# Kernel optimization log

Hardware: AMD Instinct MI355X
Metric: run time of the kernel (lower is better)

## Reference

```python
import jax, jax.numpy as jnp
from jax import lax
import numpy as np


def conv(x, w, b):
    # x: [N,C,H,W], w: [O,I,kh,kw] (torch layout), VALID padding, stride 1
    y = lax.conv_general_dilated(x, w, (1, 1), 'VALID',
                                 dimension_numbers=('NCHW', 'OIHW', 'NCHW'))
    return y + b[None, :, None, None]


def prelu4(x, a):
    return jnp.where(x > 0, x, a[None, :, None, None] * x)


def prelu1(x, a):
    return jnp.where(x > 0, x, a * x)


def maxpool_ceil(x, k, s):
    # torch MaxPool2d(k, s, ceil_mode=True): pad right/bottom so last partial window counts
    def pad_amt(n):
        out = -(-(n - k) // s) + 1  # ceil((n-k)/s)+1
        return max((out - 1) * s + k - n, 0)
    ph, pw = pad_amt(x.shape[2]), pad_amt(x.shape[3])
    return lax.reduce_window(x, -jnp.inf, lax.max, (1, 1, k, k), (1, 1, s, s),
                             [(0, 0), (0, 0), (0, ph), (0, pw)])


def setup_inputs() -> dict:
    key = jax.random.key(0)
    ks = iter(jax.random.split(key, 64))
    def rn(shape, s=0.05):
        return jax.random.normal(next(ks), shape, dtype=jnp.float32) * s
    p = {}
    p['imgs'] = rn((8, 3, 720, 720), 1.0)
    p['crops24'] = rn((2048, 3, 24, 24), 1.0)
    p['crops48'] = rn((512, 3, 48, 48), 1.0)
    # PNet
    p['pw1'] = rn((10, 3, 3, 3)); p['pb1'] = rn((10,)); p['pa1'] = jnp.full((10,), 0.25, jnp.float32)
    p['pw2'] = rn((16, 10, 3, 3)); p['pb2'] = rn((16,)); p['pa2'] = jnp.full((16,), 0.25, jnp.float32)
    p['pw3'] = rn((32, 16, 3, 3)); p['pb3'] = rn((32,)); p['pa3'] = jnp.full((32,), 0.25, jnp.float32)
    p['pw41'] = rn((2, 32, 1, 1)); p['pb41'] = rn((2,))
    p['pw42'] = rn((4, 32, 1, 1)); p['pb42'] = rn((4,))
    # RNet
    p['rw1'] = rn((28, 3, 3, 3)); p['rb1'] = rn((28,)); p['ra1'] = jnp.full((28,), 0.25, jnp.float32)
    p['rw2'] = rn((48, 28, 3, 3)); p['rb2'] = rn((48,)); p['ra2'] = jnp.full((48,), 0.25, jnp.float32)
    p['rw3'] = rn((64, 48, 2, 2)); p['rb3'] = rn((64,)); p['ra3'] = jnp.full((64,), 0.25, jnp.float32)
    p['rd4w'] = rn((128, 576)); p['rd4b'] = rn((128,)); p['ra4'] = jnp.full((128,), 0.25, jnp.float32)
    p['rd51w'] = rn((2, 128)); p['rd51b'] = rn((2,))
    p['rd52w'] = rn((4, 128)); p['rd52b'] = rn((4,))
    # ONet
    p['ow1'] = rn((32, 3, 3, 3)); p['ob1'] = rn((32,)); p['oa1'] = jnp.full((32,), 0.25, jnp.float32)
    p['ow2'] = rn((64, 32, 3, 3)); p['ob2'] = rn((64,)); p['oa2'] = jnp.full((64,), 0.25, jnp.float32)
    p['ow3'] = rn((64, 64, 3, 3)); p['ob3'] = rn((64,)); p['oa3'] = jnp.full((64,), 0.25, jnp.float32)
    p['ow4'] = rn((128, 64, 2, 2)); p['ob4'] = rn((128,)); p['oa4'] = jnp.full((128,), 0.25, jnp.float32)
    p['od5w'] = rn((256, 1152)); p['od5b'] = rn((256,)); p['oa5'] = jnp.full((256,), 0.25, jnp.float32)
    p['od61w'] = rn((2, 256)); p['od61b'] = rn((2,))
    p['od62w'] = rn((4, 256)); p['od62b'] = rn((4,))
    p['od63w'] = rn((10, 256)); p['od63b'] = rn((10,))
    return p


def reference(imgs, crops24, crops48,
              pw1, pb1, pa1, pw2, pb2, pa2, pw3, pb3, pa3, pw41, pb41, pw42, pb42,
              rw1, rb1, ra1, rw2, rb2, ra2, rw3, rb3, ra3, rd4w, rd4b, ra4,
              rd51w, rd51b, rd52w, rd52b,
              ow1, ob1, oa1, ow2, ob2, oa2, ow3, ob3, oa3, ow4, ob4, oa4,
              od5w, od5b, oa5, od61w, od61b, od62w, od62b, od63w, od63b):
    # --- PNet (fully convolutional, stage 1) ---
    x = prelu4(conv(imgs, pw1, pb1), pa1)
    x = maxpool_ceil(x, 2, 2)
    x = prelu4(conv(x, pw2, pb2), pa2)
    x = prelu4(conv(x, pw3, pb3), pa3)
    p_prob = jax.nn.softmax(conv(x, pw41, pb41), axis=1)  # [B,2,Hp,Wp]
    p_reg = conv(x, pw42, pb42)                            # [B,4,Hp,Wp]
    # --- RNet (24x24 crops, stage 2) ---
    x = prelu4(conv(crops24, rw1, rb1), ra1)
    x = maxpool_ceil(x, 3, 2)
    x = prelu4(conv(x, rw2, rb2), ra2)
    x = maxpool_ceil(x, 3, 2)
    x = prelu4(conv(x, rw3, rb3), ra3)
    x = jnp.transpose(x, (0, 3, 2, 1)).reshape(x.shape[0], -1)  # permute(0,3,2,1).view
    x = prelu1(x @ rd4w.T + rd4b, ra4)
    r_a = jax.nn.softmax(x @ rd51w.T + rd51b, axis=1)  # [N,2]
    r_b = x @ rd52w.T + rd52b                           # [N,4]
    # --- ONet (48x48 crops, stage 3) ---
    x = prelu4(conv(crops48, ow1, ob1), oa1)
    x = maxpool_ceil(x, 3, 2)
    x = prelu4(conv(x, ow2, ob2), oa2)
    x = maxpool_ceil(x, 3, 2)
    x = prelu4(conv(x, ow3, ob3), oa3)
    x = maxpool_ceil(x, 2, 2)
    x = prelu4(conv(x, ow4, ob4), oa4)
    x = jnp.transpose(x, (0, 3, 2, 1)).reshape(x.shape[0], -1)
    x = prelu1(x @ od5w.T + od5b, oa5)
    o_a = jax.nn.softmax(x @ od61w.T + od61b, axis=1)  # [M,2]
    o_b = x @ od62w.T + od62b                           # [M,4]
    o_c = x @ od63w.T + od63b                           # [M,10]
    return (p_reg, p_prob, r_b, r_a, o_b, o_c, o_a)
```

## Files before the change

### kernel.cpp

```cpp
#include <hip/hip_runtime.h>
#include <hip/hip_bf16.h>

typedef __hip_bfloat16 bf16;
typedef unsigned short u16;
typedef unsigned int u32;

typedef float f32x16 __attribute__((ext_vector_type(16)));
typedef short s16x8 __attribute__((ext_vector_type(8)));

__device__ __forceinline__ float b2f(bf16 v) { return __bfloat162float(v); }
__device__ __forceinline__ bf16  f2b(float v) { return __float2bfloat16(v); }
__device__ __forceinline__ float us2f(u16 u) { return __uint_as_float((u32)u << 16); }
__device__ __forceinline__ float ulo(u32 u)  { return __uint_as_float(u << 16); }
__device__ __forceinline__ float uhi(u32 u)  { return __uint_as_float(u & 0xFFFF0000u); }

#define OFF_IMGS 0
#define OFF_C24  12441600
#define OFF_C48  15980544
#define OFF_WTS  19519488
#define OFF_A    20119488
#define OFF_B    54819488
#define OFF_RW   71319488
#define RW_RC2   (OFF_RW)
#define RW_RC3   (OFF_RW + 18432)
#define RW_OC2   (OFF_RW + 30720)
#define RW_OC3   (OFF_RW + 49152)
#define RW_OC4   (OFF_RW + 86016)
#define ARENA_N  (OFF_RW + 118784L)

__device__ bf16 g_arena[ARENA_N];
__device__ int  g_isf32;

__global__ void detect_kern(const void* imgs)
{
    if (threadIdx.x != 0) return;
    const u16* u = (const u16*)imgs;
    int f32 = 0;
    for (int i = 0; i < 256; ++i) {
        int e = (u[i] >> 7) & 0xFF;
        if (e >= 0x8D) f32 = 1;
    }
    g_isf32 = f32;
}

__global__ void convert_kern(const void* __restrict__ src, int dst_off, int n)
{
    int i = blockIdx.x * blockDim.x + threadIdx.x;
    if (i >= n) return;
    float v = g_isf32 ? ((const float*)src)[i] : b2f(((const bf16*)src)[i]);
    g_arena[(long)dst_off + i] = f2b(v);
}

struct CvtEnt { const void* src; int dst_off; int n; };
struct CvtTab { CvtEnt e[50]; };
__global__ void convert_many_kern(CvtTab tab)
{
    CvtEnt ent = tab.e[blockIdx.y];
    int i = blockIdx.x * blockDim.x + threadIdx.x;
    if (i >= ent.n) return;
    float v = g_isf32 ? ((const float*)ent.src)[i] : b2f(((const bf16*)ent.src)[i]);
    g_arena[(long)ent.dst_off + i] = f2b(v);
}

__device__ __forceinline__ void stout(void* base, long idx, float v, int f32)
{
    if (f32) ((float*)base)[idx] = v;
    else     ((bf16*)base)[idx] = f2b(v);
}

__global__ void repack_w_kern(int w_off, int rw_off, int CO, int CIN, int CPAD,
                              int KHW, int total)
{
    int i = blockIdx.x * blockDim.x + threadIdx.x;
    if (i >= total) return;
    int c = i % CPAD;
    int t = i / CPAD;
    int g = t % KHW;
    int o = t / KHW;
    u16 v = 0;
    if (o < CO && c < CIN)
        v = ((const u16*)g_arena)[w_off + ((long)(o * CIN + c)) * KHW + g];
    ((u16*)g_arena)[(long)rw_off + i] = v;
}

template<int CIN,int KH,int KW,int H,int W,int OH,int OW,int CO,int OBLK,int R>
__launch_bounds__(256)
__global__ void conv_a_kern(int in_off, int w_off, int b_off, int a_off, int out_off)
{
    constexpr int KTOT = CIN * KH * KW;
    constexpr int INCNT = CIN * H * W;
    constexpr int OPT = OBLK / 8;
    constexpr int NPX = OH * OW;
    constexpr int PBLK = 32 * R;
    __shared__ __align__(16) u16 in_s[INCNT];
    __shared__ __align__(16) u16 w_s[KTOT * OBLK];
    __shared__ __align__(16) u16 out_s[PBLK * CO];

    int n = blockIdx.x, pxc = blockIdx.y;
    const u16* ga = (const u16*)g_arena;

    const u32* src = (const u32*)(ga + in_off + (long)n * INCNT);
    u32* dst = (u32*)in_s;
    for (int i = threadIdx.x; i < INCNT / 2; i += 256) dst[i] = src[i];
    for (int i = threadIdx.x; i < KTOT * OBLK; i += 256) {
        int o_l = i % OBLK, k = i / OBLK;
        w_s[i] = (o_l < CO) ? ga[w_off + (long)o_l * KTOT + k] : (u16)0;
    }
    __syncthreads();

    int lane = threadIdx.x & 31, og = threadIdx.x >> 5;
    int pixoff[R];
    bool vld[R];
    #pragma unroll
    for (int r = 0; r < R; ++r) {
        int px = pxc * PBLK + lane + r * 32;
        vld[r] = px < NPX;
        int p = vld[r] ? px : 0;
        pixoff[r] = (p / OW) * W + (p % OW);
    }
    float acc[R][OPT];
    #pragma unroll
    for (int r = 0; r < R; ++r)
        #pragma unroll
        for (int j = 0; j < OPT; ++j) acc[r][j] = 0.f;

    const u32* wu = (const u32*)w_s;
    for (int c = 0; c < CIN; ++c) {
        #pragma unroll
        for (int ky = 0; ky < KH; ++ky) {
            #pragma unroll
            for (int kx = 0; kx < KW; ++kx) {
                int k = (c * KH + ky) * KW + kx;
                int ub = c * (H * W) + ky * W + kx;
                float a[R];
                #pragma unroll
                for (int r = 0; r < R; ++r) a[r] = us2f(in_s[ub + pixoff[r]]);
                int wb = (k * OBLK + og * OPT) >> 1;
                float wv[OPT];
                #pragma unroll
                for (int jj = 0; jj < OPT / 2; ++jj) {
                    u32 u = wu[wb + jj];
                    wv[2 * jj] = ulo(u); wv[2 * jj + 1] = uhi(u);
                }
                #pragma unroll
                for (int r = 0; r < R; ++r)
                    #pragma unroll
                    for (int j = 0; j < OPT; ++j)
                        acc[r][j] += a[r] * wv[j];
            }
        }
    }
    #pragma unroll
    for (int j = 0; j < OPT; ++j) {
        int o = og * OPT + j;
        if (o < CO) {
            float b = us2f(ga[b_off + o]);
            float al = us2f(ga[a_off + o]);
            #pragma unroll
            for (int r = 0; r < R; ++r) if (vld[r]) {
                float v = acc[r][j] + b;
                v = v > 0.f ? v : v * al;
                u16 bits; bf16 t = f2b(v); __builtin_memcpy(&bits, &t, 2);
                out_s[(lane + r * 32) * CO + o] = bits;
            }
        }
    }
    __syncthreads();
    int base_px = pxc * PBLK;
    int npx_blk = NPX - base_px; if (npx_blk > PBLK) npx_blk = PBLK;
    int tot8 = (npx_blk * CO) >> 3;
    uint4* gout = (uint4*)&g_arena[(long)out_off + ((long)n * NPX + base_px) * CO];
    const uint4* osrc = (const uint4*)out_s;
    for (int i = threadIdx.x; i < tot8; i += 256) gout[i] = osrc[i];
}

template<int CIN,int CPAD,int KH,int KW,int H,int W,int OH,int OW,int CO,int NT>
__launch_bounds__(256, 2)
__global__ void conv_mfma_kern(int in_off, int rw_off, int b_off, int a_off, int out_off)
{
    constexpr int NPX = OH * OW;
    constexpr int MT = (NPX + 31) / 32;
    constexpr int PST = CPAD + 8;
    constexpr int NCH = CPAD / 16;
    constexpr int KHW = KH * KW;
    constexpr int NG = KHW * NCH;
    __shared__ __align__(16) u16 patchT[H * W * PST];

    int n = blockIdx.x;
    const u16* ga = (const u16*)g_arena;
    const u16* in = ga + in_off + (long)n * (H * W * CIN);

    if constexpr (CIN == CPAD) {
        constexpr int NV = H * W * (CPAD / 8);
        for (int i = threadIdx.x; i < NV; i += 256) {
            int pix = i / (CPAD / 8), j = i % (CPAD / 8);
            *(s16x8*)&patchT[pix * PST + j * 8] = *(const s16x8*)&in[pix * CPAD + j * 8];
        }
    } else {
        constexpr int TOT = H * W * CPAD;
        for (int i = threadIdx.x; i < TOT; i += 256) {
            int pix = i / CPAD, c = i % CPAD;
            patchT[pix * PST + c] = (c < CIN) ? in[pix * CIN + c] : (u16)0;
        }
    }
    __syncthreads();

    int m = threadIdx.x & 31, half = (threadIdx.x >> 5) & 1, wave = threadIdx.x >> 6;
    int c0 = half * 8;
    int nt = wave % NT;
    int o = nt * 32 + m;
    bool ovld = o < CO;
    float bb = ovld ? us2f(ga[b_off + o]) : 0.f;
    float aa = ovld ? us2f(ga[a_off + o]) : 0.f;

    s16x8 bfrag[NG];
    const u16* wb = ga + rw_off + (long)(nt * 32 + m) * (KHW * CPAD) + c0;
    #pragma unroll
    for (int g = 0; g < NG; ++g)
        bfrag[g] = *(const s16x8*)(wb + g * 16);

    for (int mt = wave / NT; mt < MT; mt += 4 / NT) {
        int p = mt * 32 + m;
        int pc = p < NPX ? p : NPX - 1;
        int pp = (pc / OW) * W + (pc % OW);
        f32x16 acc = {};
        #pragma unroll
        for (int t = 0; t < KHW; ++t) {
            int rb = (pp + (t / KW) * W + (t % KW)) * PST + c0;
            #pragma unroll
            for (int ch = 0; ch < NCH; ++ch) {
                s16x8 a = *(const s16x8*)&patchT[rb + ch * 16];
                acc = __builtin_amdgcn_mfma_f32_32x32x16_bf16(a, bfrag[t * NCH + ch], acc, 0, 0, 0);
            }
        }
        if (ovld) {
            bf16* op = g_arena + (long)out_off + (long)n * (NPX * CO) + o;
            #pragma unroll
            for (int reg = 0; reg < 16; ++reg) {
                int mrow = (reg & 3) + 8 * (reg >> 2) + 4 * half;
                int pr = mt * 32 + mrow;
                if (pr < NPX) {
                    float v = acc[reg] + bb;
                    v = v > 0.f ? v : v * aa;
                    op[(long)pr * CO] = f2b(v);
                }
            }
        }
    }
}

__launch_bounds__(256)
__global__ void pnet_c1p_kern(int w_off, int b_off, int a_off, int out_off)
{
    __shared__ u16 patch[3 * 34 * 34];
    __shared__ __align__(16) u16 w_s[27 * 16];
    int n = blockIdx.x, pty = blockIdx.y, ptx = blockIdx.z;
    int cy0 = pty * 32, cx0 = ptx * 32;
    const u16* ga = (const u16*)g_arena;

    for (int i = threadIdx.x; i < 3468; i += 256) {
        int c = i / 1156, rem = i % 1156, py = rem / 34, pxx = rem % 34;
        int iy = cy0 + py, ix = cx0 + pxx;
        u16 v = 0;
        if (iy < 720 && ix < 720)
            v = ga[OFF_IMGS + ((long)(n * 3 + c) * 720 + iy) * 720 + ix];
        patch[i] = v;
    }
    for (int i = threadIdx.x; i < 27 * 16; i += 256) {
        int o = i % 16, k = i / 16;
        w_s[i] = (o < 10) ? ga[w_off + o * 27 + k] : (u16)0;
    }
    __syncthreads();

    int px = threadIdx.x % 16, py = threadIdx.x / 16;
    float acc[2][2][10];
    #pragma unroll
    for (int a = 0; a < 2; ++a)
        #pragma unroll
        for (int b = 0; b < 2; ++b)
            #pragma unroll
            for (int o = 0; o < 10; ++o) acc[a][b][o] = 0.f;

    const uint4* wq = (const uint4*)w_s;
    for (int c = 0; c < 3; ++c) {
        #pragma unroll
        for (int ky = 0; ky < 3; ++ky) {
            #pragma unroll
            for (int kx = 0; kx < 3; ++kx) {
                int k = (c * 3 + ky) * 3 + kx;
                float a[2][2];
                #pragma unroll
                for (int dy = 0; dy < 2; ++dy)
                    #pragma unroll
                    for (int dx = 0; dx < 2; ++dx)
                        a[dy][dx] = us2f(patch[c * 1156 + (2 * py + dy + ky) * 34 + (2 * px + dx + kx)]);
                uint4 q0 = wq[k * 2], q1 = wq[k * 2 + 1];
                float wv[10];
                wv[0] = ulo(q0.x); wv[1] = uhi(q0.x); wv[2] = ulo(q0.y); wv[3] = uhi(q0.y);
                wv[4] = ulo(q0.z); wv[5] = uhi(q0.z); wv[6] = ulo(q0.w); wv[7] = uhi(q0.w);
                wv[8] = ulo(q1.x); wv[9] = uhi(q1.x);
                #pragma unroll
                for (int o = 0; o < 10; ++o)
                    #pragma unroll
                    for (int dy = 0; dy < 2; ++dy)
                        #pragma unroll
                        for (int dx = 0; dx < 2; ++dx)
                            acc[dy][dx][o] += a[dy][dx] * wv[o];
            }
        }
    }
    int pgy = pty * 16 + py, pgx = ptx * 16 + px;
    if (pgy < 359 && pgx < 359) {
        long base = ((long)n * 359 * 359 + (long)pgy * 359 + pgx) * 10;
        #pragma unroll
        for (int o = 0; o < 10; ++o) {
            float b = us2f(ga[b_off + o]);
            float al = us2f(ga[a_off + o]);
            float m = -1e30f;
            #pragma unroll
            for (int dy = 0; dy < 2; ++dy)
                #pragma unroll
                for (int dx = 0; dx < 2; ++dx) {
                    float v = acc[dy][dx][o] + b;
                    v = v > 0.f ? v : v * al;
                    m = fmaxf(m, v);
                }
            g_arena[(long)out_off + base + o] = f2b(m);
        }
    }
}

__launch_bounds__(256)
__global__ void pnet_c2m_kern(int in_off, int w_off, int b_off, int a_off, int out_off)
{
    constexpr int PST = 24;
    __shared__ __align__(16) u16 patchT[340 * PST];
    __shared__ __align__(16) u16 w2r[32 * 160];
    __shared__ float b2s[16], a2s[16];

    int n = blockIdx.x, by = blockIdx.y, tx = blockIdx.z;
    int gy0 = by * 8, gx0 = tx * 32;
    const u16* ga = (const u16*)g_arena;

    for (int i = threadIdx.x; i < 5440; i += 256) {
        int pix = i >> 4, c = i & 15;
        int py = pix / 34, pxx = pix % 34;
        int iy = gy0 + py, ix = gx0 + pxx;
        u16 v = 0;
        if (c < 10 && iy < 359 && ix < 359)
            v = ga[in_off + ((long)(n * 359 + iy) * 359 + ix) * 10 + c];
        patchT[pix * PST + c] = v;
    }
    for (int i = threadIdx.x; i < 5120; i += 256) {
        int o = i / 160, kp = i % 160;
        int g = kp >> 4, c = kp & 15;
        u16 v = 0;
        if (o < 16 && c < 10 && g < 9) v = ga[w_off + o * 90 + c * 9 + g];
        w2r[i] = v;
    }
    for (int i = threadIdx.x; i < 16; i += 256) { b2s[i] = us2f(ga[b_off + i]); a2s[i] = us2f(ga[a_off + i]); }
    __syncthreads();

    int lane = threadIdx.x & 63, w = threadIdx.x >> 6;
    int half = lane >> 5, m = lane & 31;
    int c0 = half * 8;

    s16x8 bfrag[9];
    #pragma unroll
    for (int g = 0; g < 9; ++g)
        bfrag[g] = *(const s16x8*)&w2r[m * 160 + g * 16 + c0];

    f32x16 acc0 = {}, acc1 = {};
    #pragma unroll
    for (int g = 0; g < 9; ++g) {
        int ky = g / 3, kx = g % 3;
        s16x8 a0 = *(const s16x8*)&patchT[((2 * w + 0 + ky) * 34 + m + kx) * PST + c0];
        s16x8 a1 = *(const s16x8*)&patchT[((2 * w + 1 + ky) * 34 + m + kx) * PST + c0];
        acc0 = __builtin_amdgcn_mfma_f32_32x32x16_bf16(a0, bfrag[g], acc0, 0, 0, 0);
        acc1 = __builtin_amdgcn_mfma_f32_32x32x16_bf16(a1, bfrag[g], acc1, 0, 0, 0);
    }

    if (m < 16) {
        float b = b2s[m], al = a2s[m];
        #pragma unroll
        for (int reg = 0; reg < 16; ++reg) {
            int mrow = (reg & 3) + 8 * (reg >> 2) + 4 * half;
            int gy = gy0 + 2 * w, gx = gx0 + mrow;
            if (gy < 357 && gx < 357) {
                float v = acc0[reg] + b; v = v > 0.f ? v : v * al;
                g_arena[(long)out_off + (((long)(n * 357 + gy)) * 357 + gx) * 16 + m] = f2b(v);
            }
            if (gy + 1 < 357 && gx < 357) {
                float v = acc1[reg] + b; v = v > 0.f ? v : v * al;
                g_arena[(long)out_off + (((long)(n * 357 + gy + 1)) * 357 + gx) * 16 + m] = f2b(v);
            }
        }
    }
}

__launch_bounds__(256)
__global__ void pnet_c3h_kern(int in_off, int w3o, int b3o, int a3o,
                              int w41o, int b41o, int w42o, int b42o, void* dout)
{
    constexpr int PST = 24;
    __shared__ __align__(16) u16 patchT[340 * PST];
    __shared__ __align__(16) u16 w3r[32 * 160];
    __shared__ float c3s[256 * 33];
    __shared__ float b3f[32], a3f[32], w41f[64], w42f[128], b41f[2], b42f[4];

    int n = blockIdx.x, by = blockIdx.y, tx = blockIdx.z;
    int gy0 = by * 8, gx0 = tx * 32;
    const u16* ga = (const u16*)g_arena;

    for (int i = threadIdx.x; i < 680; i += 256) {
        int pix = i >> 1, h = i & 1;
        int py = pix / 34, pxx = pix % 34;
        int iy = gy0 + py, ix = gx0 + pxx;
        s16x8 v = {};
        if (iy < 357 && ix < 357)
            v = *(const s16x8*)&ga[in_off + (((long)(n * 357 + iy)) * 357 + ix) * 16 + h * 8];
        *(s16x8*)&patchT[pix * PST + h * 8] = v;
    }
    for (int i = threadIdx.x; i < 5120; i += 256) {
        int o = i / 160, kp = i % 160;
        int g = kp >> 4, c = kp & 15;
        w3r[i] = (g < 9) ? ga[w3o + o * 144 + c * 9 + g] : (u16)0;
    }
    for (int i = threadIdx.x; i < 32; i += 256) { b3f[i] = us2f(ga[b3o + i]); a3f[i] = us2f(ga[a3o + i]); }
    for (int i = threadIdx.x; i < 64; i += 256) w41f[i] = us2f(ga[w41o + i]);
    for (int i = threadIdx.x; i < 128; i += 256) w42f[i] = us2f(ga[w42o + i]);
    if (threadIdx.x < 2) b41f[threadIdx.x] = us2f(ga[b41o + threadIdx.x]);
    if (threadIdx.x < 4) b42f[threadIdx.x] = us2f(ga[b42o + threadIdx.x]);
    __syncthreads();

    int lane = threadIdx.x & 63, w = threadIdx.x >> 6;
    int half = lane >> 5, m = lane & 31;
    int c0 = half * 8;

    s16x8 bfrag[9];
    #pragma unroll
    for (int g = 0; g < 9; ++g)
        bfrag[g] = *(const s16x8*)&w3r[m * 160 + g * 16 + c0];

    f32x16 acc0 = {}, acc1 = {};
    #pragma unroll
    for (int g = 0; g < 9; ++g) {
        int ky = g / 3, kx = g % 3;
        s16x8 a0 = *(const s16x8*)&patchT[((2 * w + 0 + ky) * 34 + m + kx) * PST + c0];
        s16x8 a1 = *(const s16x8*)&patchT[((2 * w + 1 + ky) * 34 + m + kx) * PST + c0];
        acc0 = __builtin_amdgcn_mfma_f32_32x32x16_bf16(a0, bfrag[g], acc0, 0, 0, 0);
        acc1 = __builtin_amdgcn_mfma_f32_32x32x16_bf16(a1, bfrag[g], acc1, 0, 0, 0);
    }

    {
        float b = b3f[m], al = a3f[m];
        #pragma unroll
        for (int reg = 0; reg < 16; ++reg) {
            int mrow = (reg & 3) + 8 * (reg >> 2) + 4 * half;
            float v0 = acc0[reg] + b; v0 = v0 > 0.f ? v0 : v0 * al;
            c3s[(w * 64 + mrow) * 33 + m] = v0;
            float v1 = acc1[reg] + b; v1 = v1 > 0.f ? v1 : v1 * al;
            c3s[(w * 64 + 32 + mrow) * 33 + m] = v1;
        }
    }
    __syncthreads();

    int p = threadIdx.x;
    int gy = gy0 + (p >> 5), gx = gx0 + (p & 31);
    if (gy < 355 && gx < 355) {
        int f32 = g_isf32;
        float l0 = b41f[0], l1 = b41f[1];
        float r0 = b42f[0], r1 = b42f[1], r2 = b42f[2], r3 = b42f[3];
        #pragma unroll
        for (int o = 0; o < 32; ++o) {
            float v = c3s[p * 33 + o];
            l0 += v * w41f[o];
            l1 += v * w41f[32 + o];
            r0 += v * w42f[o];
            r1 += v * w42f[32 + o];
            r2 += v * w42f[64 + o];
            r3 += v * w42f[96 + o];
        }
        float mx = fmaxf(l0, l1);
        float e0 = __expf(l0 - mx), e1 = __expf(l1 - mx);
        float inv = 1.f / (e0 + e1);
        const long HW = 355L * 355L;
        long pix = (long)gy * 355 + gx;
        stout(dout, 4032800 + ((long)n * 2 + 0) * HW + pix, e0 * inv, f32);
        stout(dout, 4032800 + ((long)n * 2 + 1) * HW + pix, e1 * inv, f32);
        stout(dout, ((long)n * 4 + 0) * HW + pix, r0, f32);
        stout(dout, ((long)n * 4 + 1) * HW + pix, r1, f32);
        stout(dout, ((long)n * 4 + 2) * HW + pix, r2, f32);
        stout(dout, ((long)n * 4 + 3) * HW + pix, r3, f32);
    }
}

__global__ void maxpool_nhwc_kern(int in_off, int out_off, int C, int H, int W,
                                  int OH, int OW, int k, int s, int total)
{
    int tid = blockIdx.x * blockDim.x + threadIdx.x;
    if (tid >= total) return;
    int c = tid % C; int t = tid / C;
    int ox = t % OW; t /= OW;
    int oy = t % OH; int n = t / OH;
    const u16* ip = (const u16*)g_arena + in_off + (long)n * H * W * C + c;
    int sy = oy * s, sx = ox * s;
    float m = -1e30f;
    for (int ky = 0; ky < k; ++ky) {
        int iy = sy + ky;
        if (iy >= H) break;
        for (int kx = 0; kx < k; ++kx) {
            int ix = sx + kx;
            if (ix >= W) break;
            m = fmaxf(m, us2f(ip[(iy * W + ix) * C]));
        }
    }
    g_arena[(long)out_off + tid] = f2b(m);
}

__global__ void flatten_hw_kern(int in_off, int out_off, int C, int H, int W, int total)
{
    int tid = blockIdx.x * blockDim.x + threadIdx.x;
    if (tid >= total) return;
    int CHW = C * H * W;
    int n = tid / CHW;
    int k = tid % CHW;
    int w = k / (H * C);
    int r = k % (H * C);
    int h = r / C;
    int c = r % C;
    g_arena[(long)out_off + tid] =
        g_arena[(long)in_off + ((long)n * H * W + h * W + w) * C + c];
}

__launch_bounds__(256)
__global__ void dense_tile_kern(int in_off, int w_off, int b_off, int a_off, int out_off,
                                int K, int J)
{
    __shared__ u16 in_s[32 * 66];
    __shared__ u16 w_s[32 * 66];
    int n0 = blockIdx.x * 32, j0 = blockIdx.y * 32;
    const u16* ga = (const u16*)g_arena;
    const u16* fin = ga + in_off;
    const u16* wts = ga + w_off;
    int sy = threadIdx.x >> 4, sx = threadIdx.x & 15;

    float acc00 = 0.f, acc01 = 0.f, acc10 = 0.f, acc11 = 0.f;

    for (int kc = 0; kc < K; kc += 64) {
        #pragma unroll
        for (int it = 0; it < 4; ++it) {
            int i = threadIdx.x + it * 256;
            int row = i >> 5, c2 = i & 31;
            u32 v = *(const u32*)(fin + (long)(n0 + row) * K + kc + c2 * 2);
            *(u32*)&in_s[row * 66 + c2 * 2] = v;
            u32 wv = *(const u32*)(wts + (long)(j0 + row) * K + kc + c2 * 2);
            *(u32*)&w_s[row * 66 + c2 * 2] = wv;
        }
        __syncthreads();
        #pragma unroll
        for (int kk = 0; kk < 64; ++kk) {
            float a0 = us2f(in_s[(2 * sy) * 66 + kk]);
            float a1 = us2f(in_s[(2 * sy + 1) * 66 + kk]);
            float b0 = us2f(w_s[(2 * sx) * 66 + kk]);
            float b1 = us2f(w_s[(2 * sx + 1) * 66 + kk]);
            acc00 += a0 * b0; acc01 += a0 * b1;
            acc10 += a1 * b0; acc11 += a1 * b1;
        }
        __syncthreads();
    }

    float accs[2][2] = {{acc00, acc01}, {acc10, acc11}};
    #pragma unroll
    for (int jj = 0; jj < 2; ++jj) {
        int j = j0 + 2 * sx + jj;
        float b = us2f(ga[b_off + j]);
        float al = us2f(ga[a_off + j]);
        #pragma unroll
        for (int ss = 0; ss < 2; ++ss) {
            int n = n0 + 2 * sy + ss;
            float v = accs[ss][jj] + b;
            v = v > 0.f ? v : v * al;
            g_arena[(long)out_off + (long)n * J + j] = f2b(v);
        }
    }
}

template<int K, int J1, int J2>
__launch_bounds__(256)
__global__ void heads_wave_kern(int fc_off, int wSo, int bSo, int w1o, int b1o,
                                int w2o, int b2o, void* dout,
                                long outS_off, long out1_off, long out2_off, int N)
{
    constexpr int KPL = K / 64;
    constexpr int NACC = 2 + J1 + J2;
    int wave = (blockIdx.x * blockDim.x + threadIdx.x) >> 6;
    int lane = threadIdx.x & 63;
    if (wave >= N) return;
    const u16* ga = (const u16*)g_arena;
    const u16* f  = ga + fc_off + (long)wave * K;
    const u16* wS = ga + wSo;
    const u16* w1 = ga + w1o;
    const u16* w2 = ga + w2o;

    float acc[NACC];
    #pragma unroll
    for (int j = 0; j < NACC; ++j) acc[j] = 0.f;

    #pragma unroll
    for (int kk = 0; kk < KPL; ++kk) {
        int k = lane + kk * 64;
        float fv = us2f(f[k]);
        acc[0] += fv * us2f(wS[k]);
        acc[1] += fv * us2f(wS[K + k]);
        #pragma unroll
        for (int j = 0; j < J1; ++j)
            acc[2 + j] += fv * us2f(w1[j * K + k]);
        #pragma unroll
        for (int j = 0; j < J2; ++j)
            acc[2 + J1 + j] += fv * us2f(w2[j * K + k]);
    }
    #pragma unroll
    for (int j = 0; j < NACC; ++j)
        #pragma unroll
        for (int off = 32; off > 0; off >>= 1)
            acc[j] += __shfl_xor(acc[j], off, 64);

    if (lane == 0) {
        int f32 = g_isf32;
        float l0 = acc[0] + us2f(ga[bSo + 0]);
        float l1 = acc[1] + us2f(ga[bSo + 1]);
        float m = fmaxf(l0, l1);
        float e0 = __expf(l0 - m), e1 = __expf(l1 - m);
        float inv = 1.f / (e0 + e1);
        stout(dout, outS_off + (long)wave * 2 + 0, e0 * inv, f32);
        stout(dout, outS_off + (long)wave * 2 + 1, e1 * inv, f32);
        #pragma unroll
        for (int j = 0; j < J1; ++j)
            stout(dout, out1_off + (long)wave * J1 + j, acc[2 + j] + us2f(ga[b1o + j]), f32);
        #pragma unroll
        for (int j = 0; j < J2; ++j)
            stout(dout, out2_off + (long)wave * J2 + j, acc[2 + J1 + j] + us2f(ga[b2o + j]), f32);
    }
}

static inline dim3 g1(int total) { return dim3((unsigned)((total + 255) / 256)); }

extern "C" void kernel_launch(void* const* d_in, const int* in_sizes, int n_in,
                              void* d_out, int out_size, void* d_ws, size_t ws_size,
                              hipStream_t stream)
{
    int woff[53];
    int acc = OFF_WTS;
    int mx = 0;
    for (int i = 3; i < 53; ++i) { woff[i] = acc; acc += in_sizes[i]; if (in_sizes[i] > mx) mx = in_sizes[i]; }

    detect_kern<<<1, 64, 0, stream>>>(d_in[0]);
    convert_kern<<<g1(12441600), 256, 0, stream>>>(d_in[0], OFF_IMGS, 12441600);
    convert_kern<<<g1(3538944), 256, 0, stream>>>(d_in[1], OFF_C24, 3538944);
    convert_kern<<<g1(3538944), 256, 0, stream>>>(d_in[2], OFF_C48, 3538944);
    CvtTab tab;
    for (int i = 3; i < 53; ++i) tab.e[i - 3] = CvtEnt{ d_in[i], woff[i], in_sizes[i] };
    convert_many_kern<<<dim3((unsigned)((mx + 255) / 256), 50), 256, 0, stream>>>(tab);

    repack_w_kern<<<g1(18432), 256, 0, stream>>>(woff[19], RW_RC2, 48, 28, 32, 9, 18432);
    repack_w_kern<<<g1(12288), 256, 0, stream>>>(woff[22], RW_RC3, 64, 48, 48, 4, 12288);
    repack_w_kern<<<g1(18432), 256, 0, stream>>>(woff[35], RW_OC2, 64, 32, 32, 9, 18432);
    repack_w_kern<<<g1(36864), 256, 0, stream>>>(woff[38], RW_OC3, 64, 64, 64, 9, 36864);
    repack_w_kern<<<g1(32768), 256, 0, stream>>>(woff[41], RW_OC4, 128, 64, 64, 4, 32768);

    pnet_c1p_kern<<<dim3(8, 23, 23), 256, 0, stream>>>(woff[3], woff[4], woff[5], OFF_A);
    pnet_c2m_kern<<<dim3(8, 45, 12), 256, 0, stream>>>(OFF_A, woff[6], woff[7], woff[8], OFF_B);
    pnet_c3h_kern<<<dim3(8, 45, 12), 256, 0, stream>>>(OFF_B,
        woff[9], woff[10], woff[11], woff[12], woff[13], woff[14], woff[15], d_out);

    conv_a_kern<3,3,3,24,24,22,22,28,32,4><<<dim3(2048, 4, 1), 256, 0, stream>>>(
        OFF_C24, woff[16], woff[17], woff[18], OFF_A);
    maxpool_nhwc_kern<<<g1(6938624), 256, 0, stream>>>(OFF_A, OFF_B, 28, 22, 22, 11, 11, 3, 2, 6938624);
    conv_mfma_kern<28,32,3,3,11,11,9,9,48,2><<<dim3(2048), 256, 0, stream>>>(
        OFF_B, RW_RC2, woff[20], woff[21], OFF_A);
    maxpool_nhwc_kern<<<g1(1572864), 256, 0, stream>>>(OFF_A, OFF_B, 48, 9, 9, 4, 4, 3, 2, 1572864);
    conv_mfma_kern<48,48,2,2,4,4,3,3,64,2><<<dim3(2048), 256, 0, stream>>>(
        OFF_B, RW_RC3, woff[23], woff[24], OFF_A);
    flatten_hw_kern<<<g1(1179648), 256, 0, stream>>>(OFF_A, OFF_B, 64, 3, 3, 1179648);
    dense_tile_kern<<<dim3(64, 4), 256, 0, stream>>>(OFF_B, woff[25], woff[26], woff[27], OFF_A,
        576, 128);
    heads_wave_kern<128,4,0><<<dim3(512), 256, 0, stream>>>(OFF_A,
        woff[28], woff[29], woff[30], woff[31], 0, 0,
        d_out, 6057392L, 6049200L, 0L, 2048);

    conv_a_kern<3,3,3,48,48,46,46,32,32,4><<<dim3(512, 17, 1), 256, 0, stream>>>(
        OFF_C48, woff[32], woff[33], woff[34], OFF_A);
    maxpool_nhwc_kern<<<g1(8667136), 256, 0, stream>>>(OFF_A, OFF_B, 32, 46, 46, 23, 23, 3, 2, 8667136);
    conv_mfma_kern<32,32,3,3,23,23,21,21,64,2><<<dim3(512), 256, 0, stream>>>(
        OFF_B, RW_OC2, woff[36], woff[37], OFF_A);
    maxpool_nhwc_kern<<<g1(3276800), 256, 0, stream>>>(OFF_A, OFF_B, 64, 21, 21, 10, 10, 3, 2, 3276800);
    conv_mfma_kern<64,64,3,3,10,10,8,8,64,2><<<dim3(512), 256, 0, stream>>>(
        OFF_B, RW_OC3, woff[39], woff[40], OFF_A);
    maxpool_nhwc_kern<<<g1(524288), 256, 0, stream>>>(OFF_A, OFF_B, 64, 8, 8, 4, 4, 2, 2, 524288);
    conv_mfma_kern<64,64,2,2,4,4,3,3,128,4><<<dim3(512), 256, 0, stream>>>(
        OFF_B, RW_OC4, woff[42], woff[43], OFF_A);
    flatten_hw_kern<<<g1(589824), 256, 0, stream>>>(OFF_A, OFF_B, 128, 3, 3, 589824);
    dense_tile_kern<<<dim3(16, 8), 256, 0, stream>>>(OFF_B, woff[44], woff[45], woff[46], OFF_A,
        1152, 256);
    heads_wave_kern<256,4,10><<<dim3(128), 256, 0, stream>>>(OFF_A,
        woff[47], woff[48], woff[49], woff[50], woff[51], woff[52],
        d_out, 6068656L, 6061488L, 6063536L, 512);
}
```

Measured before the change: 968.8 us.

## Move PNet conv1 to bf16 MFMA with NHWC image conversion

The image conversion kernel now transposes the NCHW input into an NHWC bf16 layout. PNet's first conv plus PReLU plus 2x2 max-pool is rewritten to use 32x32x16 bf16 MFMA instructions, with channels padded to 16 and 9 tap groups. This replaces the scalar FMA loop that produced 10 channels. The trade-offs are that most of the MFMA work goes on zero padding (3 of 16 channels, 10 of 32 outputs), the conversion pass does strided reads, and the grid is larger.

```diff
diff --git a/kernel.cpp b/kernel.cpp
--- a/kernel.cpp
+++ b/kernel.cpp
@@ -48,6 +48,21 @@
     int i = blockIdx.x * blockDim.x + threadIdx.x;
     if (i >= n) return;
     float v = g_isf32 ? ((const float*)src)[i] : b2f(((const bf16*)src)[i]);
+    g_arena[(long)dst_off + i] = f2b(v);
+}
+
+__global__ void convert_img_kern(const void* __restrict__ src, int dst_off, int n)
+{
+    int i = blockIdx.x * blockDim.x + threadIdx.x;
+    if (i >= n) return;
+    int c = i % 3;
+    int t = i / 3;
+    int x = t % 720;
+    int t2 = t / 720;
+    int y = t2 % 720;
+    int nn = t2 / 720;
+    long si = ((long)(nn * 3 + c) * 720 + y) * 720 + x;
+    float v = g_isf32 ? ((const float*)src)[si] : b2f(((const bf16*)src)[si]);
     g_arena[(long)dst_off + i] = f2b(v);
 }
 
@@ -250,82 +265,79 @@
 }
 
 __launch_bounds__(256)
-__global__ void pnet_c1p_kern(int w_off, int b_off, int a_off, int out_off)
-{
-    __shared__ u16 patch[3 * 34 * 34];
-    __shared__ __align__(16) u16 w_s[27 * 16];
-    int n = blockIdx.x, pty = blockIdx.y, ptx = blockIdx.z;
-    int cy0 = pty * 32, cx0 = ptx * 32;
+__global__ void pnet_c1m_kern(int w_off, int b_off, int a_off, int out_off)
+{
+    constexpr int PST = 24;
+    __shared__ __align__(16) u16 patchT[612 * PST];
+    __shared__ __align__(16) u16 w1r[32 * 160];
+    __shared__ float b1s[16], a1s[16];
+
+    int n = blockIdx.x, by = blockIdx.y, tx = blockIdx.z;
+    int gy0 = by * 16, gx0 = tx * 32;
     const u16* ga = (const u16*)g_arena;
 
-    for (int i = threadIdx.x; i < 3468; i += 256) {
-        int c = i / 1156, rem = i % 1156, py = rem / 34, pxx = rem % 34;
-        int iy = cy0 + py, ix = cx0 + pxx;
+    for (int i = threadIdx.x; i < 612 * 16; i += 256) {
+        int pix = i >> 4, c = i & 15;
+        int py = pix / 34, pxx = pix % 34;
+        int iy = gy0 + py, ix = gx0 + pxx;
         u16 v = 0;
-        if (iy < 720 && ix < 720)
-            v = ga[OFF_IMGS + ((long)(n * 3 + c) * 720 + iy) * 720 + ix];
-        patch[i] = v;
-    }
-    for (int i = threadIdx.x; i < 27 * 16; i += 256) {
-        int o = i % 16, k = i / 16;
-        w_s[i] = (o < 10) ? ga[w_off + o * 27 + k] : (u16)0;
+        if (c < 3 && iy < 720 && ix < 720)
+            v = ga[OFF_IMGS + (((long)n * 720 + iy) * 720 + ix) * 3 + c];
+        patchT[pix * PST + c] = v;
+    }
+    for (int i = threadIdx.x; i < 5120; i += 256) {
+        int o = i / 160, kp = i % 160;
+        int g = kp >> 4, c = kp & 15;
+        u16 v = 0;
+        if (o < 10 && c < 3 && g < 9) v = ga[w_off + o * 27 + c * 9 + g];
+        w1r[i] = v;
+    }
+    for (int i = threadIdx.x; i < 16; i += 256) {
+        b1s[i] = (i < 10) ? us2f(ga[b_off + i]) : 0.f;
+        a1s[i] = (i < 10) ? us2f(ga[a_off + i]) : 0.f;
     }
     __syncthreads();
 
-    int px = threadIdx.x % 16, py = threadIdx.x / 16;
-    float acc[2][2][10];
-    #pragma unroll
-    for (int a = 0; a < 2; ++a)
-        #pragma unroll
-        for (int b = 0; b < 2; ++b)
-            #pragma unroll
-            for (int o = 0; o < 10; ++o) acc[a][b][o] = 0.f;
-
-    const uint4* wq = (const uint4*)w_s;
-    for (int c = 0; c < 3; ++c) {
-        #pragma unroll
-        for (int ky = 0; ky < 3; ++ky) {
-            #pragma unroll
-            for (int kx = 0; kx < 3; ++kx) {
-                int k = (c * 3 + ky) * 3 + kx;
-                float a[2][2];
+    int lane = threadIdx.x & 63, w = threadIdx.x >> 6;
+    int half = lane >> 5, m = lane & 31;
+    int c0 = half * 8;
+
+    s16x8 bfrag[9];
+    #pragma unroll
+    for (int g = 0; g < 9; ++g)
+        bfrag[g] = *(const s16x8*)&w1r[m * 160 + g * 16 + c0];
+
+    f32x16 acc[4] = {};
+    #pragma unroll
+    for (int g = 0; g < 9; ++g) {
+        int ky = g / 3, kx = g % 3;
+        #pragma unroll
+        for (int rj = 0; rj < 4; ++rj) {
+            s16x8 a = *(const s16x8*)&patchT[((4 * w + rj + ky) * 34 + m + kx) * PST + c0];
+            acc[rj] = __builtin_amdgcn_mfma_f32_32x32x16_bf16(a, bfrag[g], acc[rj], 0, 0, 0);
+        }
+    }
+
+    if (m < 10) {
+        float b = b1s[m], al = a1s[m];
+        #pragma unroll
+        for (int s = 0; s < 2; ++s) {
+            int pr = by * 8 + 2 * w + s;
+            if (pr < 359) {
                 #pragma unroll
-                for (int dy = 0; dy < 2; ++dy)
-                    #pragma unroll
-                    for (int dx = 0; dx < 2; ++dx)
-                        a[dy][dx] = us2f(patch[c * 1156 + (2 * py + dy + ky) * 34 + (2 * px + dx + kx)]);
-                uint4 q0 = wq[k * 2], q1 = wq[k * 2 + 1];
-                float wv[10];
-                wv[0] = ulo(q0.x); wv[1] = uhi(q0.x); wv[2] = ulo(q0.y); wv[3] = uhi(q0.y);
-                wv[4] = ulo(q0.z); wv[5] = uhi(q0.z); wv[6] = ulo(q0.w); wv[7] = uhi(q0.w);
-                wv[8] = ulo(q1.x); wv[9] = uhi(q1.x);
-                #pragma unroll
-                for (int o = 0; o < 10; ++o)
-                    #pragma unroll
-                    for (int dy = 0; dy < 2; ++dy)
-                        #pragma unroll
-                        for (int dx = 0; dx < 2; ++dx)
-                            acc[dy][dx][o] += a[dy][dx] * wv[o];
+                for (int u = 0; u < 8; ++u) {
+                    int pxo = (u & 1) + 4 * (u >> 1) + 2 * half;
+                    int px = tx * 16 + pxo;
+                    if (px < 359) {
+                        float v0 = acc[2 * s][2 * u] + b;     v0 = v0 > 0.f ? v0 : v0 * al;
+                        float v1 = acc[2 * s][2 * u + 1] + b; v1 = v1 > 0.f ? v1 : v1 * al;
+                        float v2 = acc[2 * s + 1][2 * u] + b;     v2 = v2 > 0.f ? v2 : v2 * al;
+                        float v3 = acc[2 * s + 1][2 * u + 1] + b; v3 = v3 > 0.f ? v3 : v3 * al;
+                        float mx = fmaxf(fmaxf(v0, v1), fmaxf(v2, v3));
+                        g_arena[(long)out_off + (((long)n * 359 + pr) * 359 + px) * 10 + m] = f2b(mx);
+                    }
+                }
             }
-        }
-    }
-    int pgy = pty * 16 + py, pgx = ptx * 16 + px;
-    if (pgy < 359 && pgx < 359) {
-        long base = ((long)n * 359 * 359 + (long)pgy * 359 + pgx) * 10;
-        #pragma unroll
-        for (int o = 0; o < 10; ++o) {
-            float b = us2f(ga[b_off + o]);
-            float al = us2f(ga[a_off + o]);
-            float m = -1e30f;
-            #pragma unroll
-            for (int dy = 0; dy < 2; ++dy)
-                #pragma unroll
-                for (int dx = 0; dx < 2; ++dx) {
-                    float v = acc[dy][dx][o] + b;
-                    v = v > 0.f ? v : v * al;
-                    m = fmaxf(m, v);
-                }
-            g_arena[(long)out_off + base + o] = f2b(m);
         }
     }
 }
@@ -656,7 +668,7 @@
     for (int i = 3; i < 53; ++i) { woff[i] = acc; acc += in_sizes[i]; if (in_sizes[i] > mx) mx = in_sizes[i]; }
 
     detect_kern<<<1, 64, 0, stream>>>(d_in[0]);
-    convert_kern<<<g1(12441600), 256, 0, stream>>>(d_in[0], OFF_IMGS, 12441600);
+    convert_img_kern<<<g1(12441600), 256, 0, stream>>>(d_in[0], OFF_IMGS, 12441600);
     convert_kern<<<g1(3538944), 256, 0, stream>>>(d_in[1], OFF_C24, 3538944);
     convert_kern<<<g1(3538944), 256, 0, stream>>>(d_in[2], OFF_C48, 3538944);
     CvtTab tab;
@@ -669,7 +681,7 @@
     repack_w_kern<<<g1(36864), 256, 0, stream>>>(woff[38], RW_OC3, 64, 64, 64, 9, 36864);
     repack_w_kern<<<g1(32768), 256, 0, stream>>>(woff[41], RW_OC4, 128, 64, 64, 4, 32768);
 
-    pnet_c1p_kern<<<dim3(8, 23, 23), 256, 0, stream>>>(woff[3], woff[4], woff[5], OFF_A);
+    pnet_c1m_kern<<<dim3(8, 45, 23), 256, 0, stream>>>(woff[3], woff[4], woff[5], OFF_A);
     pnet_c2m_kern<<<dim3(8, 45, 12), 256, 0, stream>>>(OFF_A, woff[6], woff[7], woff[8], OFF_B);
     pnet_c3h_kern<<<dim3(8, 45, 12), 256, 0, stream>>>(OFF_B,
         woff[9], woff[10], woff[11], woff[12], woff[13], woff[14], woff[15], d_out);
```

After: 1.023 ms. 5.6% more time.
